# Kernel tuning notes

Hardware: AMD Instinct MI355X
Metric: run time of the kernel (lower is better)

The kernel has to match this reference:

```python
import jax, jax.numpy as jnp
import numpy as np

N_HEADS = 16
NEG_INF = -1e9


def _apply_rope(xq, xk, cos, sin):
    # xq, xk: [B, S, H, hd]; cos/sin: [S, hd//2]
    def rot(t):
        B, S, H, hd = t.shape
        t = t.reshape(B, S, H, hd // 2, 2)
        t0, t1 = t[..., 0], t[..., 1]
        c = cos[None, :, None, :]
        s = sin[None, :, None, :]
        o0 = t0 * c - t1 * s
        o1 = t0 * s + t1 * c
        return jnp.stack([o0, o1], axis=-1).reshape(B, S, H, hd)
    return rot(xq), rot(xk)


def setup_inputs() -> dict:
    key = jax.random.key(0)
    ks = jax.random.split(key, 7)
    B, S, D = 2, 2048, 2048
    hd = D // N_HEADS
    return {
        "x": jax.random.normal(ks[0], (B, S, D), dtype=jnp.float32),
        "freqs_cos": jax.random.uniform(ks[1], (S, hd // 2), dtype=jnp.float32),
        "freqs_sin": jax.random.uniform(ks[2], (S, hd // 2), dtype=jnp.float32),
        "wq": jax.random.normal(ks[3], (D, D), dtype=jnp.float32) * 0.02,
        "wk": jax.random.normal(ks[4], (D, D), dtype=jnp.float32) * 0.02,
        "wv": jax.random.normal(ks[5], (D, D), dtype=jnp.float32) * 0.02,
        "wo": jax.random.normal(ks[6], (D, D), dtype=jnp.float32) * 0.02,
    }


def reference(x, freqs_cos, freqs_sin, wq, wk, wv, wo):
    B, S, D = x.shape
    H = N_HEADS
    hd = D // H

    # projections (torch Linear: y = x @ W.T)
    xq = (x @ wq.T).reshape(B, S, H, hd)
    xk = (x @ wk.T).reshape(B, S, H, hd)
    xv = (x @ wv.T).reshape(B, S, H, hd)

    xq, xk = _apply_rope(xq, xk, freqs_cos, freqs_sin)

    # [B, H, S, hd]
    q = xq.transpose(0, 2, 1, 3)
    k = xk.transpose(0, 2, 1, 3)
    v = xv.transpose(0, 2, 1, 3)

    scores = jnp.einsum("bhqd,bhkd->bhqk", q, k) / jnp.sqrt(jnp.float32(hd))
    causal = jnp.triu(jnp.full((S, S), NEG_INF, dtype=scores.dtype), k=1)
    scores = scores + causal[None, None]
    probs = jax.nn.softmax(scores.astype(jnp.float32), axis=-1).astype(q.dtype)

    out = jnp.einsum("bhqk,bhkd->bhqd", probs, v)
    out = out.transpose(0, 2, 1, 3).reshape(B, S, D)
    return out @ wo.T
```

## Files before the change

kernel.cpp:

```cpp
#include <hip/hip_runtime.h>
#include <hip/hip_bf16.h>
#include <math.h>

typedef __attribute__((ext_vector_type(8))) short short8;
typedef __attribute__((ext_vector_type(4))) short short4v;
typedef __attribute__((ext_vector_type(4))) float f32x4;
typedef unsigned short ushort_t;

__device__ __forceinline__ ushort_t f2bf(float f) {
    union { float f; unsigned u; } v; v.f = f;
    unsigned r = v.u + 0x7FFF + ((v.u >> 16) & 1);
    return (ushort_t)(r >> 16);
}
__device__ __forceinline__ float bf2f(short s) {
    union { unsigned u; float f; } v; v.u = ((unsigned)(ushort_t)s) << 16;
    return v.f;
}

__global__ void cvt_all(const float* __restrict__ x,
                        const float* __restrict__ w0, const float* __restrict__ w1,
                        const float* __restrict__ w2, const float* __restrict__ w3,
                        ushort_t* __restrict__ dst, int md8, int dd8) {
    int i = blockIdx.x * blockDim.x + threadIdx.x;
    int stride = gridDim.x * blockDim.x;
    const int total = md8 + 4 * dd8;
    for (; i < total; i += stride) {
        const float* src;
        long off;
        if (i < md8) { src = x; off = i; }
        else {
            int j = i - md8;
            int which = j / dd8;
            off = j - (long)which * dd8;
            src = (which == 0) ? w0 : (which == 1) ? w1 : (which == 2) ? w2 : w3;
        }
        const float4* s = reinterpret_cast<const float4*>(src) + off * 2;
        float4 a = s[0], b = s[1];
        short8 o;
        o[0] = (short)f2bf(a.x); o[1] = (short)f2bf(a.y);
        o[2] = (short)f2bf(a.z); o[3] = (short)f2bf(a.w);
        o[4] = (short)f2bf(b.x); o[5] = (short)f2bf(b.y);
        o[6] = (short)f2bf(b.z); o[7] = (short)f2bf(b.w);
        reinterpret_cast<short8*>(dst)[i] = o;
    }
}

__global__ __launch_bounds__(512, 2) void gemm256_qkv(const ushort_t* __restrict__ A,
                                                      const ushort_t* __restrict__ Bw,
                                                      ushort_t* __restrict__ Cout,
                                                      ushort_t* __restrict__ Vt,
                                                      const float* __restrict__ fc,
                                                      const float* __restrict__ fs,
                                                      int M, int N, int K) {
    extern __shared__ __align__(16) ushort_t lds[];
    ushort_t* As = lds;
    ushort_t* Bs = lds + 32768;
    const int t = threadIdx.x;
    const int wid = t >> 6, lane = t & 63;
    const int wr = wid >> 2, wc = wid & 3;
    const int lr = lane & 15, lg = lane >> 4;

    const int ntc = N >> 8;
    const int nwg = (M >> 8) * ntc;
    const int bid = blockIdx.y * gridDim.x + blockIdx.x;
    const int cpx = nwg >> 3;
    const int swz = (bid & 7) * cpx + (bid >> 3);
    const int m0 = (swz / ntc) * 256, n0 = (swz % ntc) * 256;

    f32x4 acc[8][4] = {};

    const int r0 = t >> 3;
    const int c0 = (t & 7) ^ (r0 & 7);
    const ushort_t* gA = A + (long)(m0 + r0) * K + c0 * 8;
    const ushort_t* gB = Bw + (long)(n0 + r0) * K + c0 * 8;

    int aoffE[2];
    aoffE[0] = lr * 64 + (((0 + lg) ^ (lr & 7)) << 3);
    aoffE[1] = lr * 64 + (((4 + lg) ^ (lr & 7)) << 3);

    const int nt = K >> 6;

#define STAGE_A(X, h) do { const int p_ = (X) & 1;                                             \
    __builtin_amdgcn_global_load_lds((const __attribute__((address_space(1))) unsigned int*)   \
        (gA + (long)((h) * 128) * K + (X) * 64),                                               \
        (__attribute__((address_space(3))) unsigned int*)(As + (p_ * 2 + (h)) * 8192 + t * 8), \
        16, 0, 0);                                                                             \
    __builtin_amdgcn_global_load_lds((const __attribute__((address_space(1))) unsigned int*)   \
        (gA + (long)((h) * 128 + 64) * K + (X) * 64),                                          \
        (__attribute__((address_space(3))) unsigned int*)(As + (p_ * 2 + (h)) * 8192 + 4096 + t * 8), \
        16, 0, 0); } while (0)

#define STAGE_B(X, h) do { const int p_ = (X) & 1;                                             \
    __builtin_amdgcn_global_load_lds((const __attribute__((address_space(1))) unsigned int*)   \
        (gB + (long)((h) * 128) * K + (X) * 64),                                               \
        (__attribute__((address_space(3))) unsigned int*)(Bs + (p_ * 2 + (h)) * 8192 + t * 8), \
        16, 0, 0);                                                                             \
    __builtin_amdgcn_global_load_lds((const __attribute__((address_space(1))) unsigned int*)   \
        (gB + (long)((h) * 128 + 64) * K + (X) * 64),                                          \
        (__attribute__((address_space(3))) unsigned int*)(Bs + (p_ * 2 + (h)) * 8192 + 4096 + t * 8), \
        16, 0, 0); } while (0)

#define MIDSYNC() do {                                             \
    asm volatile("" ::: "memory");                                 \
    __builtin_amdgcn_s_barrier();                                  \
    asm volatile("s_waitcnt lgkmcnt(0)" ::: "memory");             \
    __builtin_amdgcn_sched_barrier(0); } while (0)

#define ENDBAR() do {                                              \
    asm volatile("" ::: "memory");                                 \
    __builtin_amdgcn_s_barrier(); } while (0)

#define MFMA_Q(AROW, BCOL, AR, BR) do {                            \
    __builtin_amdgcn_s_setprio(1);                                 \
    _Pragma("unroll")                                              \
    for (int ks = 0; ks < 2; ++ks)                                 \
        _Pragma("unroll")                                          \
        for (int m = 0; m < 4; ++m)                                \
            _Pragma("unroll")                                      \
            for (int n = 0; n < 2; ++n)                            \
                acc[(AROW) + m][(BCOL) + n] =                      \
                    __builtin_amdgcn_mfma_f32_16x16x32_bf16((AR)[m][ks], (BR)[n][ks], acc[(AROW) + m][(BCOL) + n], 0, 0, 0); \
    __builtin_amdgcn_s_setprio(0); } while (0)

#define KTILE(U, BUF) do {                                                                     \
    const int Asb = ((BUF) * 2 + wr) * 8192;                                                   \
    const int Bcb = ((BUF) * 2 + (wc >> 1)) * 8192 + (wc & 1) * 4096;                          \
    _Pragma("unroll")                                                                          \
    for (int m = 0; m < 4; ++m)                                                                \
        _Pragma("unroll")                                                                      \
        for (int ks = 0; ks < 2; ++ks)                                                         \
            ar[m][ks] = *reinterpret_cast<const short8*>(&As[Asb + m * 1024 + aoffE[ks]]);     \
    _Pragma("unroll")                                                                          \
    for (int n = 0; n < 2; ++n)                                                                \
        _Pragma("unroll")                                                                      \
        for (int ks = 0; ks < 2; ++ks)                                                         \
            br0[n][ks] = *reinterpret_cast<const short8*>(&Bs[Bcb + n * 1024 + aoffE[ks]]);    \
    if ((U) + 1 < nt) STAGE_A((U) + 1, 1);                                                     \
    MIDSYNC();                                                                                 \
    MFMA_Q(0, 0, ar, br0);                                                                     \
    ENDBAR();                                                                                  \
    _Pragma("unroll")                                                                          \
    for (int n = 0; n < 2; ++n)                                                                \
        _Pragma("unroll")                                                                      \
        for (int ks = 0; ks < 2; ++ks)                                                         \
            br1[n][ks] = *reinterpret_cast<const short8*>(&Bs[Bcb + 2048 + n * 1024 + aoffE[ks]]); \
    MIDSYNC();                                                                                 \
    MFMA_Q(0, 2, ar, br1);                                                                     \
    ENDBAR();                                                                                  \
    _Pragma("unroll")                                                                          \
    for (int m = 0; m < 4; ++m)                                                                \
        _Pragma("unroll")                                                                      \
        for (int ks = 0; ks < 2; ++ks)                                                         \
            ar[m][ks] = *reinterpret_cast<const short8*>(&As[Asb + 4096 + m * 1024 + aoffE[ks]]); \
    if ((U) + 2 < nt) STAGE_B((U) + 2, 0);                                                     \
    MIDSYNC();                                                                                 \
    MFMA_Q(4, 2, ar, br1);                                                                     \
    ENDBAR();                                                                                  \
    if ((U) + 2 < nt) { STAGE_A((U) + 2, 0); STAGE_B((U) + 2, 1); }                            \
    asm volatile("" ::: "memory");                                                             \
    __builtin_amdgcn_s_barrier();                                                              \
    MFMA_Q(4, 0, ar, br0);                                                                     \
    if ((U) < nt - 2) {                                                                        \
        asm volatile("s_waitcnt vmcnt(6)" ::: "memory");                                       \
    } else if ((U) == nt - 2) {                                                                \
        asm volatile("s_waitcnt vmcnt(0)" ::: "memory");                                       \
    }                                                                                          \
    __builtin_amdgcn_s_barrier(); } while (0)

    STAGE_A(0, 0); STAGE_A(0, 1); STAGE_B(0, 0); STAGE_B(0, 1);
    STAGE_A(1, 0); STAGE_B(1, 0); STAGE_B(1, 1);
    asm volatile("s_waitcnt vmcnt(6)" ::: "memory");
    __builtin_amdgcn_s_barrier();

    short8 ar[4][2], br0[2][2], br1[2][2];

    for (int U = 0; U < nt; U += 2) {
        KTILE(U, 0);
        KTILE(U + 1, 1);
    }
#undef KTILE
#undef MFMA_Q
#undef ENDBAR
#undef MIDSYNC
#undef STAGE_A
#undef STAGE_B

    const int S = 2048;
    #pragma unroll
    for (int m = 0; m < 8; ++m) {
        #pragma unroll
        for (int n = 0; n < 4; ++n) {
            const int col = n0 + wc * 64 + n * 16 + lr;
            const int which = col >> 11;
            const int h = (col >> 7) & 15;
            const int d = col & 127;
            const int rowb = m0 + wr * 128 + m * 16 + lg * 4;
            const int bb = rowb >> 11;
            const int sb = rowb & 2047;
            if (which == 2) {
                short4v o;
                #pragma unroll
                for (int r = 0; r < 4; ++r) o[r] = (short)f2bf(acc[m][n][r]);
                *reinterpret_cast<short4v*>(Vt + ((long)(bb * 16 + h) * 128 + d) * S + sb) = o;
            } else {
                const int i0 = d >> 1;
                #pragma unroll
                for (int r = 0; r < 4; ++r) {
                    const int s = sb + r;
                    float v = acc[m][n][r];
                    float p = __shfl_xor(v, 1);
                    float c  = fc[(long)s * 64 + i0];
                    float sn = fs[(long)s * 64 + i0];
                    float o = (lr & 1) ? (p * sn + v * c) : (v * c - p * sn);
                    Cout[(long)which * M * 2048 + (((long)(bb * 16 + h)) * 2048 + s) * 128 + d] = f2bf(o);
                }
            }
        }
    }
}

__global__ __launch_bounds__(256) void gemm_nt_f32(const ushort_t* __restrict__ A,
                                                   const ushort_t* __restrict__ Bw,
                                                   float* __restrict__ Cout,
                                                   int M, int N, int K) {
    __shared__ __align__(16) ushort_t As[2 * 128 * 32];
    __shared__ __align__(16) ushort_t Bs[2 * 128 * 32];
    const int t = threadIdx.x;
    const int wid = t >> 6, lane = t & 63;
    const int wm = wid >> 1, wn = wid & 1;
    const int lr = lane & 15, lg = lane >> 4;

    const int ntc = N >> 7;
    const int nwg = (M >> 7) * ntc;
    const int bid = blockIdx.y * gridDim.x + blockIdx.x;
    const int cpx = nwg >> 3;
    const int swz = (bid & 7) * cpx + (bid >> 3);
    const int m0 = (swz / ntc) * 128, n0 = (swz % ntc) * 128;

    f32x4 acc[4][4] = {};

    const int sh0 = wid * 1024 + lane * 8;
    const int sh1 = sh0 + 512;
    const int r0 = sh0 >> 5, c0 = sh0 & 31;
    const int r1 = sh1 >> 5, c1 = sh1 & 31;

    const ushort_t* gA0 = A + (long)(m0 + r0) * K + c0;
    const ushort_t* gA1 = A + (long)(m0 + r1) * K + c1;
    const ushort_t* gB0 = Bw + (long)(n0 + r0) * K + c0;
    const ushort_t* gB1 = Bw + (long)(n0 + r1) * K + c1;

    auto stage = [&](int k0, int nb) {
        ushort_t* as = As + nb * 4096;
        ushort_t* bs = Bs + nb * 4096;
        __builtin_amdgcn_global_load_lds((const __attribute__((address_space(1))) unsigned int*)(gA0 + k0),
                                         (__attribute__((address_space(3))) unsigned int*)(as + sh0), 16, 0, 0);
        __builtin_amdgcn_global_load_lds((const __attribute__((address_space(1))) unsigned int*)(gA1 + k0),
                                         (__attribute__((address_space(3))) unsigned int*)(as + sh1), 16, 0, 0);
        __builtin_amdgcn_global_load_lds((const __attribute__((address_space(1))) unsigned int*)(gB0 + k0),
                                         (__attribute__((address_space(3))) unsigned int*)(bs + sh0), 16, 0, 0);
        __builtin_amdgcn_global_load_lds((const __attribute__((address_space(1))) unsigned int*)(gB1 + k0),
                                         (__attribute__((address_space(3))) unsigned int*)(bs + sh1), 16, 0, 0);
    };

    const int nt = K >> 5;
    stage(0, 0);
    __syncthreads();
    int cur = 0;

    for (int ti = 0; ti < nt; ++ti) {
        if (ti + 1 < nt) stage((ti + 1) << 5, cur ^ 1);
        const ushort_t* as = As + cur * 4096;
        const ushort_t* bs = Bs + cur * 4096;
        short8 af[4], bfr[4];
        #pragma unroll
        for (int m = 0; m < 4; ++m)
            af[m] = *reinterpret_cast<const short8*>(&as[(wm * 64 + m * 16 + lr) * 32 + lg * 8]);
        #pragma unroll
        for (int n = 0; n < 4; ++n)
            bfr[n] = *reinterpret_cast<const short8*>(&bs[(wn * 64 + n * 16 + lr) * 32 + lg * 8]);
        #pragma unroll
        for (int m = 0; m < 4; ++m)
            #pragma unroll
            for (int n = 0; n < 4; ++n)
                acc[m][n] = __builtin_amdgcn_mfma_f32_16x16x32_bf16(af[m], bfr[n], acc[m][n], 0, 0, 0);
        __syncthreads();
        cur ^= 1;
    }

    #pragma unroll
    for (int m = 0; m < 4; ++m) {
        #pragma unroll
        for (int n = 0; n < 4; ++n) {
            const int col = n0 + wn * 64 + n * 16 + lr;
            #pragma unroll
            for (int r = 0; r < 4; ++r) {
                const int row = m0 + wm * 64 + m * 16 + lg * 4 + r;
                Cout[(long)row * N + col] = acc[m][n][r];
            }
        }
    }
}

__global__ __launch_bounds__(256, 3) void attn_kernel(const ushort_t* __restrict__ Qp,
                                                      const ushort_t* __restrict__ Kp,
                                                      const ushort_t* __restrict__ Vtg,
                                                      ushort_t* __restrict__ O,
                                                      int S, int H) {
    __shared__ __align__(16) ushort_t Ks[64][136];
    __shared__ __align__(16) ushort_t Vs[128][72];
    __shared__ __align__(16) ushort_t Pl[4][16][72];
    const int t = threadIdx.x, wid = t >> 6, lane = t & 63;
    const int lr = lane & 15, lg = lane >> 4;
    const int bh = blockIdx.y;
    const int b = bh / H, h = bh % H;
    const ushort_t* Qh = Qp + (long)bh * S * 128;
    const ushort_t* Kh = Kp + (long)bh * S * 128;
    const ushort_t* Vth = Vtg + (long)bh * 128 * S;
    const int nq = S / 64;
    const float scale = 0.08838834764831845f;

    const int ksr = t >> 2;
    const int ksc = (t & 3) * 32;
    const int vsr = t & 127;
    const int vsc = (t >> 7) * 32;

    for (int qsel = 0; qsel < 2; ++qsel) {
        const int qt = qsel ? (nq - 1 - blockIdx.x) : blockIdx.x;
        const int qb0 = qt * 64;

        const int qrow = qb0 + wid * 16 + lr;
        short8 qf[4];
        #pragma unroll
        for (int kk = 0; kk < 4; ++kk)
            qf[kk] = *reinterpret_cast<const short8*>(Qh + (long)qrow * 128 + kk * 32 + lg * 8);

        f32x4 oacc[8] = {};
        float mrow[4], lsum[4];
        #pragma unroll
        for (int r = 0; r < 4; ++r) { mrow[r] = -INFINITY; lsum[r] = 0.f; }

        const int nkt = qt + 1;

        short8 kreg[4], vreg[4];
        {
            const ushort_t* kgp = Kh + t * 32;
            const ushort_t* vgp = Vth + (long)vsr * S + vsc;
            #pragma unroll
            for (int j = 0; j < 4; ++j) kreg[j] = *reinterpret_cast<const short8*>(kgp + j * 8);
            #pragma unroll
            for (int j = 0; j < 4; ++j) vreg[j] = *reinterpret_cast<const short8*>(vgp + j * 8);
        }

        for (int kt = 0; kt < nkt; ++kt) {
            const int kv0 = kt * 64;
            __syncthreads();
            #pragma unroll
            for (int j = 0; j < 4; ++j)
                *reinterpret_cast<short8*>(&Ks[ksr][ksc + j * 8]) = kreg[j];
            #pragma unroll
            for (int j = 0; j < 4; ++j)
                *reinterpret_cast<short8*>(&Vs[vsr][vsc + j * 8]) = vreg[j];
            __syncthreads();
            if (kt + 1 < nkt) {
                const ushort_t* kgp = Kh + (long)(kv0 + 64) * 128 + t * 32;
                const ushort_t* vgp = Vth + (long)vsr * S + kv0 + 64 + vsc;
                #pragma unroll
                for (int j = 0; j < 4; ++j) kreg[j] = *reinterpret_cast<const short8*>(kgp + j * 8);
                #pragma unroll
                for (int j = 0; j < 4; ++j) vreg[j] = *reinterpret_cast<const short8*>(vgp + j * 8);
            }

            f32x4 sacc[4] = {};
            #pragma unroll
            for (int kk = 0; kk < 4; ++kk) {
                #pragma unroll
                for (int n = 0; n < 4; ++n) {
                    short8 kf = *reinterpret_cast<const short8*>(&Ks[n * 16 + lr][kk * 32 + lg * 8]);
                    sacc[n] = __builtin_amdgcn_mfma_f32_16x16x32_bf16(qf[kk], kf, sacc[n], 0, 0, 0);
                }
            }
            float sv[4][4];
            const int myq = qb0 + wid * 16 + lg * 4;
            #pragma unroll
            for (int n = 0; n < 4; ++n) {
                int kcol = kv0 + n * 16 + lr;
                #pragma unroll
                for (int r = 0; r < 4; ++r) {
                    float xv = sacc[n][r] * scale;
                    sv[n][r] = (kcol > myq + r) ? -1e9f : xv;
                }
            }
            float alpha[4];
            #pragma unroll
            for (int r = 0; r < 4; ++r) {
                float mx = fmaxf(fmaxf(sv[0][r], sv[1][r]), fmaxf(sv[2][r], sv[3][r]));
                #pragma unroll
                for (int off = 1; off < 16; off <<= 1)
                    mx = fmaxf(mx, __shfl_xor(mx, off));
                float mnew = fmaxf(mrow[r], mx);
                alpha[r] = __expf(mrow[r] - mnew);
                float ts = 0.f;
                #pragma unroll
                for (int n = 0; n < 4; ++n) {
                    float p = __expf(sv[n][r] - mnew);
                    sv[n][r] = p;
                    ts += p;
                }
                #pragma unroll
                for (int off = 1; off < 16; off <<= 1)
                    ts += __shfl_xor(ts, off);
                lsum[r] = lsum[r] * alpha[r] + ts;
                mrow[r] = mnew;
            }
            #pragma unroll
            for (int f = 0; f < 8; ++f)
                #pragma unroll
                for (int r = 0; r < 4; ++r)
                    oacc[f][r] *= alpha[r];
            #pragma unroll
            for (int n = 0; n < 4; ++n)
                #pragma unroll
                for (int r = 0; r < 4; ++r)
                    Pl[wid][lg * 4 + r][n * 16 + lr] = f2bf(sv[n][r]);
            __asm volatile("" ::: "memory");
            short8 pf[2];
            #pragma unroll
            for (int ks = 0; ks < 2; ++ks)
                pf[ks] = *reinterpret_cast<const short8*>(&Pl[wid][lr][ks * 32 + lg * 8]);
            #pragma unroll
            for (int ks = 0; ks < 2; ++ks) {
                #pragma unroll
                for (int f = 0; f < 8; ++f) {
                    short8 vf = *reinterpret_cast<const short8*>(&Vs[f * 16 + lr][ks * 32 + lg * 8]);
                    oacc[f] = __builtin_amdgcn_mfma_f32_16x16x32_bf16(pf[ks], vf, oacc[f], 0, 0, 0);
                }
            }
        }
        float inv[4];
        #pragma unroll
        for (int r = 0; r < 4; ++r) inv[r] = 1.f / lsum[r];
        ushort_t* Oh = O + (long)b * S * 2048 + h * 128;
        #pragma unroll
        for (int f = 0; f < 8; ++f) {
            #pragma unroll
            for (int r = 0; r < 4; ++r) {
                int row = qb0 + wid * 16 + lg * 4 + r;
                int col = f * 16 + lr;
                Oh[(long)row * 2048 + col] = f2bf(oacc[f][r] * inv[r]);
            }
        }
    }
}

extern "C" void kernel_launch(void* const* d_in, const int* in_sizes, int n_in,
                              void* d_out, int out_size, void* d_ws, size_t ws_size,
                              hipStream_t stream) {
    const float* x  = (const float*)d_in[0];
    const float* fc = (const float*)d_in[1];
    const float* fs = (const float*)d_in[2];
    const float* wq = (const float*)d_in[3];
    const float* wk = (const float*)d_in[4];
    const float* wv = (const float*)d_in[5];
    const float* wo = (const float*)d_in[6];
    float* out = (float*)d_out;

    const int B = 2, S = 2048, D = 2048, H = 16;
    const int M = B * S;
    const size_t MD = (size_t)M * D;
    const size_t DD = (size_t)D * D;

    char* ws = (char*)d_ws;
    ushort_t* xbf = (ushort_t*)ws;
    ushort_t* wqb = (ushort_t*)(ws + MD * 2);
    ushort_t* wob = wqb + 3 * DD;
    ushort_t* qp  = wqb + 4 * DD;
    ushort_t* kp  = qp + MD;
    ushort_t* vtg = kp + MD;
    ushort_t* attnb = xbf;

    cvt_all<<<2048, 256, 0, stream>>>(x, wq, wk, wv, wo, xbf, (int)(MD / 8), (int)(DD / 8));

    dim3 gq(6144 / 256, M / 256);
    gemm256_qkv<<<gq, 512, 131072, stream>>>(xbf, wqb, qp, vtg, fc, fs, M, 3 * D, D);

    dim3 ga(S / 128, B * H);
    attn_kernel<<<ga, 256, 0, stream>>>(qp, kp, vtg, attnb, S, H);

    dim3 gg(D / 128, M / 128);
    gemm_nt_f32<<<gg, 256, 0, stream>>>(attnb, wob, out, M, D, D);
}
```

Measured before the change: 306.5 us.

## Swizzle attention LDS tiles, lazy softmax rescale, interleave RoPE cos/sin

Replaces the padded K/V shared-memory tiles in the attention kernel with unpadded XOR-swizzled layouts, so the short8 fragment reads avoid bank conflicts while using less LDS. Adds a lazy online-softmax path: when the new row max stays within 8 of the running max across the whole wavefront, the kernel skips the max update and the rescaling of the output accumulators. The conversion kernel now also packs the RoPE cos and sin tables into interleaved float2 pairs, so the QKV epilogue fetches both with one load. The lazy path lets exponentials reach about e^8 before normalization, which slightly changes numerics, and the extra packing pass adds a little work to the conversion kernel.

Result: slower. 437.9 us (+42.9%).

```diff
diff --git a/kernel.cpp b/kernel.cpp
--- a/kernel.cpp
+++ b/kernel.cpp
@@ -20,28 +20,42 @@
 __global__ void cvt_all(const float* __restrict__ x,
                         const float* __restrict__ w0, const float* __restrict__ w1,
                         const float* __restrict__ w2, const float* __restrict__ w3,
-                        ushort_t* __restrict__ dst, int md8, int dd8) {
+                        const float* __restrict__ fc, const float* __restrict__ fs,
+                        ushort_t* __restrict__ dst, float2* __restrict__ fcs,
+                        int md8, int dd8, int npair4) {
     int i = blockIdx.x * blockDim.x + threadIdx.x;
     int stride = gridDim.x * blockDim.x;
-    const int total = md8 + 4 * dd8;
+    const int total0 = md8 + 4 * dd8;
+    const int total = total0 + npair4;
     for (; i < total; i += stride) {
-        const float* src;
-        long off;
-        if (i < md8) { src = x; off = i; }
-        else {
-            int j = i - md8;
-            int which = j / dd8;
-            off = j - (long)which * dd8;
-            src = (which == 0) ? w0 : (which == 1) ? w1 : (which == 2) ? w2 : w3;
+        if (i < total0) {
+            const float* src;
+            long off;
+            if (i < md8) { src = x; off = i; }
+            else {
+                int j = i - md8;
+                int which = j / dd8;
+                off = j - (long)which * dd8;
+                src = (which == 0) ? w0 : (which == 1) ? w1 : (which == 2) ? w2 : w3;
+            }
+            const float4* s = reinterpret_cast<const float4*>(src) + off * 2;
+            float4 a = s[0], b = s[1];
+            short8 o;
+            o[0] = (short)f2bf(a.x); o[1] = (short)f2bf(a.y);
+            o[2] = (short)f2bf(a.z); o[3] = (short)f2bf(a.w);
+            o[4] = (short)f2bf(b.x); o[5] = (short)f2bf(b.y);
+            o[6] = (short)f2bf(b.z); o[7] = (short)f2bf(b.w);
+            reinterpret_cast<short8*>(dst)[i] = o;
+        } else {
+            int j = i - total0;
+            float4 c4 = reinterpret_cast<const float4*>(fc)[j];
+            float4 s4 = reinterpret_cast<const float4*>(fs)[j];
+            float2* o = fcs + (long)j * 4;
+            o[0] = make_float2(c4.x, s4.x);
+            o[1] = make_float2(c4.y, s4.y);
+            o[2] = make_float2(c4.z, s4.z);
+            o[3] = make_float2(c4.w, s4.w);
         }
-        const float4* s = reinterpret_cast<const float4*>(src) + off * 2;
-        float4 a = s[0], b = s[1];
-        short8 o;
-        o[0] = (short)f2bf(a.x); o[1] = (short)f2bf(a.y);
-        o[2] = (short)f2bf(a.z); o[3] = (short)f2bf(a.w);
-        o[4] = (short)f2bf(b.x); o[5] = (short)f2bf(b.y);
-        o[6] = (short)f2bf(b.z); o[7] = (short)f2bf(b.w);
-        reinterpret_cast<short8*>(dst)[i] = o;
     }
 }
 
@@ -49,8 +63,7 @@
                                                       const ushort_t* __restrict__ Bw,
                                                       ushort_t* __restrict__ Cout,
                                                       ushort_t* __restrict__ Vt,
-                                                      const float* __restrict__ fc,
-                                                      const float* __restrict__ fs,
+                                                      const float2* __restrict__ fcs,
                                                       int M, int N, int K) {
     extern __shared__ __align__(16) ushort_t lds[];
     ushort_t* As = lds;
@@ -209,9 +222,8 @@
                     const int s = sb + r;
                     float v = acc[m][n][r];
                     float p = __shfl_xor(v, 1);
-                    float c  = fc[(long)s * 64 + i0];
-                    float sn = fs[(long)s * 64 + i0];
-                    float o = (lr & 1) ? (p * sn + v * c) : (v * c - p * sn);
+                    float2 cs = fcs[(long)s * 64 + i0];
+                    float o = (lr & 1) ? (p * cs.y + v * cs.x) : (v * cs.x - p * cs.y);
                     Cout[(long)which * M * 2048 + (((long)(bb * 16 + h)) * 2048 + s) * 128 + d] = f2bf(o);
                 }
             }
@@ -306,8 +318,8 @@
                                                       const ushort_t* __restrict__ Vtg,
                                                       ushort_t* __restrict__ O,
                                                       int S, int H) {
-    __shared__ __align__(16) ushort_t Ks[64][136];
-    __shared__ __align__(16) ushort_t Vs[128][72];
+    __shared__ __align__(16) ushort_t Ks[64 * 128];
+    __shared__ __align__(16) ushort_t Vs[128 * 64];
     __shared__ __align__(16) ushort_t Pl[4][16][72];
     const int t = threadIdx.x, wid = t >> 6, lane = t & 63;
     const int lr = lane & 15, lg = lane >> 4;
@@ -320,7 +332,6 @@
     const float scale = 0.08838834764831845f;
 
     const int ksr = t >> 2;
-    const int ksc = (t & 3) * 32;
     const int vsr = t & 127;
     const int vsc = (t >> 7) * 32;
 
@@ -356,10 +367,10 @@
             __syncthreads();
             #pragma unroll
             for (int j = 0; j < 4; ++j)
-                *reinterpret_cast<short8*>(&Ks[ksr][ksc + j * 8]) = kreg[j];
+                *reinterpret_cast<short8*>(&Ks[(ksr << 7) + (((((t & 3) << 2) + j) ^ (ksr & 7)) << 3)]) = kreg[j];
             #pragma unroll
             for (int j = 0; j < 4; ++j)
-                *reinterpret_cast<short8*>(&Vs[vsr][vsc + j * 8]) = vreg[j];
+                *reinterpret_cast<short8*>(&Vs[(vsr << 6) + (((((t >> 7) << 2) + j) ^ (vsr & 7)) << 3)]) = vreg[j];
             __syncthreads();
             if (kt + 1 < nkt) {
                 const ushort_t* kgp = Kh + (long)(kv0 + 64) * 128 + t * 32;
@@ -375,7 +386,8 @@
             for (int kk = 0; kk < 4; ++kk) {
                 #pragma unroll
                 for (int n = 0; n < 4; ++n) {
-                    short8 kf = *reinterpret_cast<const short8*>(&Ks[n * 16 + lr][kk * 32 + lg * 8]);
+                    short8 kf = *reinterpret_cast<const short8*>(
+                        &Ks[((n * 16 + lr) << 7) + ((((kk << 2) + lg) ^ (lr & 7)) << 3)]);
                     sacc[n] = __builtin_amdgcn_mfma_f32_16x16x32_bf16(qf[kk], kf, sacc[n], 0, 0, 0);
                 }
             }
@@ -390,33 +402,57 @@
                     sv[n][r] = (kcol > myq + r) ? -1e9f : xv;
                 }
             }
-            float alpha[4];
+            float mx[4];
             #pragma unroll
             for (int r = 0; r < 4; ++r) {
-                float mx = fmaxf(fmaxf(sv[0][r], sv[1][r]), fmaxf(sv[2][r], sv[3][r]));
+                float m_ = fmaxf(fmaxf(sv[0][r], sv[1][r]), fmaxf(sv[2][r], sv[3][r]));
                 #pragma unroll
                 for (int off = 1; off < 16; off <<= 1)
-                    mx = fmaxf(mx, __shfl_xor(mx, off));
-                float mnew = fmaxf(mrow[r], mx);
-                alpha[r] = __expf(mrow[r] - mnew);
-                float ts = 0.f;
-                #pragma unroll
-                for (int n = 0; n < 4; ++n) {
-                    float p = __expf(sv[n][r] - mnew);
-                    sv[n][r] = p;
-                    ts += p;
+                    m_ = fmaxf(m_, __shfl_xor(m_, off));
+                mx[r] = m_;
+            }
+            int ok = (mx[0] <= mrow[0] + 8.f) && (mx[1] <= mrow[1] + 8.f) &&
+                     (mx[2] <= mrow[2] + 8.f) && (mx[3] <= mrow[3] + 8.f);
+            if (__all(ok)) {
+                #pragma unroll
+                for (int r = 0; r < 4; ++r) {
+                    float ts = 0.f;
+                    #pragma unroll
+                    for (int n = 0; n < 4; ++n) {
+                        float p = __expf(sv[n][r] - mrow[r]);
+                        sv[n][r] = p;
+                        ts += p;
+                    }
+                    #pragma unroll
+                    for (int off = 1; off < 16; off <<= 1)
+                        ts += __shfl_xor(ts, off);
+                    lsum[r] += ts;
                 }
-                #pragma unroll
-                for (int off = 1; off < 16; off <<= 1)
-                    ts += __shfl_xor(ts, off);
-                lsum[r] = lsum[r] * alpha[r] + ts;
-                mrow[r] = mnew;
-            }
-            #pragma unroll
-            for (int f = 0; f < 8; ++f)
-                #pragma unroll
-                for (int r = 0; r < 4; ++r)
-                    oacc[f][r] *= alpha[r];
+            } else {
+                float alpha[4];
+                #pragma unroll
+                for (int r = 0; r < 4; ++r) {
+                    float mnew = fmaxf(mrow[r], mx[r]);
+                    alpha[r] = __expf(mrow[r] - mnew);
+                    float ts = 0.f;
+                    #pragma unroll
+                    for (int n = 0; n < 4; ++n) {
+                        float p = __expf(sv[n][r] - mnew);
+                        sv[n][r] = p;
+                        ts += p;
+                    }
+                    #pragma unroll
+                    for (int off = 1; off < 16; off <<= 1)
+                        ts += __shfl_xor(ts, off);
+                    lsum[r] = lsum[r] * alpha[r] + ts;
+                    mrow[r] = mnew;
+                }
+                #pragma unroll
+                for (int f = 0; f < 8; ++f)
+                    #pragma unroll
+                    for (int r = 0; r < 4; ++r)
+                        oacc[f][r] *= alpha[r];
+            }
             #pragma unroll
             for (int n = 0; n < 4; ++n)
                 #pragma unroll
@@ -431,7 +467,8 @@
             for (int ks = 0; ks < 2; ++ks) {
                 #pragma unroll
                 for (int f = 0; f < 8; ++f) {
-                    short8 vf = *reinterpret_cast<const short8*>(&Vs[f * 16 + lr][ks * 32 + lg * 8]);
+                    short8 vf = *reinterpret_cast<const short8*>(
+                        &Vs[((f * 16 + lr) << 6) + ((((ks << 2) + lg) ^ (lr & 7)) << 3)]);
                     oacc[f] = __builtin_amdgcn_mfma_f32_16x16x32_bf16(pf[ks], vf, oacc[f], 0, 0, 0);
                 }
             }
@@ -476,12 +513,15 @@
     ushort_t* qp  = wqb + 4 * DD;
     ushort_t* kp  = qp + MD;
     ushort_t* vtg = kp + MD;
+    float2* fcs   = (float2*)(vtg + MD);
     ushort_t* attnb = xbf;
 
-    cvt_all<<<2048, 256, 0, stream>>>(x, wq, wk, wv, wo, xbf, (int)(MD / 8), (int)(DD / 8));
+    const int npair4 = S * 64 / 4;
+    cvt_all<<<2048, 256, 0, stream>>>(x, wq, wk, wv, wo, fc, fs, xbf, fcs,
+                                      (int)(MD / 8), (int)(DD / 8), npair4);
 
     dim3 gq(6144 / 256, M / 256);
-    gemm256_qkv<<<gq, 512, 131072, stream>>>(xbf, wqb, qp, vtg, fc, fs, M, 3 * D, D);
+    gemm256_qkv<<<gq, 512, 131072, stream>>>(xbf, wqb, qp, vtg, fcs, M, 3 * D, D);
 
     dim3 ga(S / 128, B * H);
     attn_kernel<<<ga, 256, 0, stream>>>(qp, kp, vtg, attnb, S, H);
```
